# Optimization experiments

Measured on AMD Instinct MI355X. Metric: run time of the kernel, lower is better.

The kernel has to match this reference:

```python
import jax, jax.numpy as jnp
import numpy as np

B, D, H, E = 1024, 64, 128, 8192


def setup_inputs() -> dict:
    key = jax.random.key(0)
    ks = jax.random.split(key, 10)
    def w(k, shape, fan_in):
        return jax.random.normal(k, shape, jnp.float32) / np.float32(np.sqrt(fan_in))
    return {
        "mu": jax.random.normal(ks[0], (B, D), jnp.float32),
        "current_edge_index": jax.random.randint(ks[1], (2, E), 0, B),
        "W1": w(ks[2], (D, H), D),   "b1": jnp.zeros((H,), jnp.float32),
        "W2": w(ks[3], (H, H), H),   "b2": jnp.zeros((H,), jnp.float32),
        "Ws1": w(ks[4], (2 * H, H), 2 * H), "bs1": jnp.zeros((H,), jnp.float32),
        "Ws2": w(ks[5], (H, 1), H),  "bs2": jnp.zeros((1,), jnp.float32),
        "Wg1": w(ks[6], (2 * H, H), 2 * H), "bg1": jnp.zeros((H,), jnp.float32),
        "Wg2": w(ks[7], (H, D), H), "bg2": jnp.zeros((D,), jnp.float32),
    }


def _gcn(x, W, b, src, dst, n):
    loop = jnp.arange(n)
    s = jnp.concatenate([src, loop])
    d = jnp.concatenate([dst, loop])
    deg = jax.ops.segment_sum(jnp.ones_like(s, x.dtype), d, num_segments=n)
    dinv = jax.lax.rsqrt(jnp.maximum(deg, 1e-12))
    norm = dinv[s] * dinv[d]                      # [E+n]
    xw = x @ W                                    # [n,H]
    out = jax.ops.segment_sum(xw[s] * norm[:, None], d, num_segments=n)
    return out + b


def _pairwise_scores(h, Ws1, bs1, Ws2, bs2):
    # score_mlp([h_i || h_j]) for all pairs, vectorized: split first-layer weight
    A = h @ Ws1[:H]                               # [B,H] contribution of h_i
    C = h @ Ws1[H:]                               # [B,H] contribution of h_j
    pre = jax.nn.relu(A[:, None, :] + C[None, :, :] + bs1)   # [B,B,H]
    s = (pre @ Ws2)[..., 0] + bs2[0]              # [B,B]
    up = jnp.triu(s, 1)                           # only i<j computed in original
    return up + up.T                              # symmetric, zero diagonal


def _kruskal(scores_np, n):
    iu, ju = np.triu_indices(n, 1)
    w = scores_np[iu, ju]
    order = np.argsort(-w, kind="stable")         # descending, stable like list.sort
    parent = list(range(n))
    rank = [0] * n
    def find(u):
        while parent[u] != u:
            parent[u] = parent[parent[u]]
            u = parent[u]
        return u
    edges = []
    for k in order:
        i, j = int(iu[k]), int(ju[k])
        ri, rj = find(i), find(j)
        if ri == rj:
            continue
        if rank[ri] < rank[rj]:
            parent[ri] = rj
        elif rank[ri] > rank[rj]:
            parent[rj] = ri
        else:
            parent[rj] = ri
            rank[ri] += 1
        edges.append((i, j))
        if len(edges) == n - 1:
            break
    return np.asarray(edges, dtype=np.int64)      # [n-1, 2]


def reference(mu, current_edge_index, W1, b1, W2, b2, Ws1, bs1, Ws2, bs2, Wg1, bg1, Wg2, bg2):
    src, dst = current_edge_index[0], current_edge_index[1]
    h = jax.nn.relu(_gcn(mu, W1, b1, src, dst, B))
    h = jax.nn.relu(_gcn(h, W2, b2, src, dst, B))
    scores = _pairwise_scores(h, Ws1, bs1, Ws2, bs2)          # [B,B]
    mst = _kruskal(np.asarray(scores), B)                     # [B-1,2], i<j
    ei = jnp.asarray(mst[:, 0])
    ej = jnp.asarray(mst[:, 1])
    # bidirectional edge index: src=[i,j,...], dst=[j,i,...]
    new_edge_index = jnp.stack([
        jnp.stack([ei, ej], axis=1).reshape(-1),
        jnp.stack([ej, ei], axis=1).reshape(-1),
    ], axis=0)                                                # [2, 2*(B-1)]
    hp = jnp.concatenate([h[ei], h[ej]], axis=1)              # [B-1, 2H]
    gamma = jnp.tanh(jax.nn.relu(hp @ Wg1 + bg1) @ Wg2 + bg2) # [B-1, D]
    return (new_edge_index, gamma)
```

## Files before the change

### kernel.cpp

```cpp
#include <hip/hip_runtime.h>
#include <hip/hip_bf16.h>
#include <math.h>

#define BN 1024
#define DIN 64
#define HD 128
#define EN 8192
#define SLOTS_STRIDE 64
#define MMR4 4
#define EGR 8
#define NC 128

typedef unsigned long long u64;

__global__ void k_fill(const int* dst, int* cnt, int* slots) {
    int e = blockIdx.x * blockDim.x + threadIdx.x;
    if (e < EN) {
        int d = dst[e];
        int p = atomicAdd(&cnt[d], 1);
        if (p < SLOTS_STRIDE) slots[d * SLOTS_STRIDE + p] = e;
    }
}

__global__ __launch_bounds__(128) void k_finish(int* slots, const int* cnt, float* dinv) {
    __shared__ int buf[128][65];
    int tid = threadIdx.x;
    int t = blockIdx.x * 128 + tid;
    int n = cnt[t];
    if (n > SLOTS_STRIDE) n = SLOTS_STRIDE;
    for (int k = 0; k < n; k++) buf[tid][k] = slots[t * SLOTS_STRIDE + k];
    for (int k = 1; k < n; k++) {
        int v = buf[tid][k];
        int q = k - 1;
        while (q >= 0 && buf[tid][q] > v) { buf[tid][q + 1] = buf[tid][q]; q--; }
        buf[tid][q + 1] = v;
    }
    for (int k = 0; k < n; k++) slots[t * SLOTS_STRIDE + k] = buf[tid][k];
    dinv[t] = 1.0f / sqrtf(fmaxf((float)(n + 1), 1e-12f));
}

__global__ __launch_bounds__(256) void k_mm4(const float* x, const float* W, const float* bias,
                                             float* out, int K) {
    __shared__ float xr[MMR4][HD];
    int tid = threadIdx.x;
    int r0 = blockIdx.x * MMR4;
    for (int idx = tid; idx < MMR4 * K; idx += 256)
        xr[idx / K][idx % K] = x[r0 * K + idx];
    __syncthreads();
    int col = tid & 127, half = tid >> 7;
    float b = bias ? bias[col] : 0.0f;
    float a0 = b, a1 = b;
#pragma unroll 4
    for (int k = 0; k < K; k++) {
        float w = W[k * HD + col];
        a0 = fmaf(xr[half * 2 + 0][k], w, a0);
        a1 = fmaf(xr[half * 2 + 1][k], w, a1);
    }
    out[(r0 + half * 2 + 0) * HD + col] = a0;
    out[(r0 + half * 2 + 1) * HD + col] = a1;
}

__global__ __launch_bounds__(256) void k_mmAC(const float* h, const float* Ws1, const float* bs1,
                                              float* Aa, float* Cc) {
    __shared__ float xr[MMR4][HD];
    int tid = threadIdx.x;
    int r0 = blockIdx.x * MMR4;
    for (int idx = tid; idx < MMR4 * HD; idx += 256)
        xr[idx >> 7][idx & 127] = h[r0 * HD + idx];
    __syncthreads();
    int col = tid & 127, half = tid >> 7;
    float bc = bs1[col];
    float A0 = 0.0f, A1 = 0.0f, C0 = bc, C1 = bc;
#pragma unroll 2
    for (int k = 0; k < HD; k++) {
        float wa = Ws1[k * HD + col];
        float wc = Ws1[(HD + k) * HD + col];
        A0 = fmaf(xr[half * 2 + 0][k], wa, A0);
        A1 = fmaf(xr[half * 2 + 1][k], wa, A1);
        C0 = fmaf(xr[half * 2 + 0][k], wc, C0);
        C1 = fmaf(xr[half * 2 + 1][k], wc, C1);
    }
    Aa[(r0 + half * 2 + 0) * HD + col] = A0;
    Aa[(r0 + half * 2 + 1) * HD + col] = A1;
    Cc[(r0 + half * 2 + 0) * HD + col] = C0;
    Cc[(r0 + half * 2 + 1) * HD + col] = C1;
}

__global__ __launch_bounds__(128) void k_gather(const float* xw, const float* bvec, const int* src,
                                                const int* slots, const int* cnt,
                                                const float* dinv, float* hout) {
    __shared__ int sn_s[SLOTS_STRIDE];
    __shared__ float w_s[SLOTS_STRIDE];
    int d = blockIdx.x, t = threadIdx.x;
    float dd = dinv[d];
    int n = cnt[d];
    if (n > SLOTS_STRIDE) n = SLOTS_STRIDE;
    if (t < n) {
        int e = slots[d * SLOTS_STRIDE + t];
        int sn = src[e];
        sn_s[t] = sn;
        w_s[t] = dinv[sn] * dd;
    }
    __syncthreads();
    float acc = 0.0f;
    for (int s = 0; s < n; s++)
        acc = fmaf(xw[sn_s[s] * HD + t], w_s[s], acc);
    acc = fmaf(xw[d * HD + t], dd * dd, acc);
    acc += bvec[t];
    hout[d * HD + t] = fmaxf(acc, 0.0f);
}

__device__ __forceinline__ u64 edge_key(float w, int i, int j) {
    unsigned u = __float_as_uint(w);
    u = (u & 0x80000000u) ? ~u : (u | 0x80000000u);
    int a = i < j ? i : j, b = i < j ? j : i;
    unsigned packed = (unsigned)(a * BN + b);
    return ((u64)u << 20) | (u64)(0xFFFFFu - packed);
}

__global__ __launch_bounds__(256) void k_scores(const float* Aa, const float* Cc,
                                                const float* Ws2, const float* bs2v,
                                                float* S, u64* best) {
    int bid = blockIdx.x;
    int bi = 0, rem = bid;
    while (rem >= 16 - bi) { rem -= 16 - bi; bi++; }
    int bj = bi + rem;
    __shared__ float As[64][68];
    __shared__ float Cs[64][68];
    __shared__ float w2[HD];
    __shared__ u64 rmax[64], cmax[64];
    int tid = threadIdx.x;
    int R = bi * 64, Cb = bj * 64;
    if (tid < HD) w2[tid] = Ws2[tid];
    if (tid < 64) { rmax[tid] = 0ull; cmax[tid] = 0ull; }
    int tx = tid & 15, ty = tid >> 4;
    float acc[4][4] = {};
    for (int half = 0; half < 2; half++) {
        int k0 = half * 64;
        __syncthreads();
        for (int idx = tid; idx < 64 * 64; idx += 256) {
            int row = idx >> 6;
            int kk = idx & 63;
            As[kk][row] = Aa[(R + row) * HD + k0 + kk];
            Cs[kk][row] = Cc[(Cb + row) * HD + k0 + kk];
        }
        __syncthreads();
        for (int kk = 0; kk < 64; kk++) {
            float4 av = *(const float4*)&As[kk][ty * 4];
            float4 cv = *(const float4*)&Cs[kk][tx * 4];
            float wk = w2[k0 + kk];
            float ar[4] = {av.x, av.y, av.z, av.w};
            float cr[4] = {cv.x, cv.y, cv.z, cv.w};
#pragma unroll
            for (int r = 0; r < 4; r++)
#pragma unroll
                for (int q = 0; q < 4; q++) {
                    float tv = fmaxf(ar[r] + cr[q], 0.0f);
                    acc[r][q] = fmaf(tv, wk, acc[r][q]);
                }
        }
    }
    float b2 = bs2v[0];
    u64 rloc[4] = {0ull, 0ull, 0ull, 0ull};
    u64 cloc[4] = {0ull, 0ull, 0ull, 0ull};
#pragma unroll
    for (int r = 0; r < 4; r++)
#pragma unroll
        for (int q = 0; q < 4; q++) {
            int gr = R + ty * 4 + r, gc = Cb + tx * 4 + q;
            float v = acc[r][q] + b2;
            if (gr < gc) {
                S[gr * BN + gc] = v;
                S[gc * BN + gr] = v;
                u64 key = edge_key(v, gr, gc);
                if (key > rloc[r]) rloc[r] = key;
                if (key > cloc[q]) cloc[q] = key;
            } else if (gr == gc) S[gr * BN + gc] = 0.0f;
        }
#pragma unroll
    for (int r = 0; r < 4; r++) {
        if (rloc[r]) atomicMax(&rmax[ty * 4 + r], rloc[r]);
        if (cloc[r]) atomicMax(&cmax[tx * 4 + r], cloc[r]);
    }
    __syncthreads();
    if (tid < 64) {
        if (rmax[tid]) atomicMax(&best[R + tid], rmax[tid]);
    } else if (tid < 128) {
        if (cmax[tid - 64]) atomicMax(&best[Cb + tid - 64], cmax[tid - 64]);
    }
}

__global__ __launch_bounds__(256) void k_best(const float* S, const int* comp,
                                              u64* best, const int* mstcnt,
                                              const int* ncompG, int ncGuard) {
    if (*mstcnt >= BN - 1) return;
    if (ncGuard && *ncompG <= NC) return;
    int lane = threadIdx.x & 63;
    int i = blockIdx.x * 4 + (threadIdx.x >> 6);
    int ci = comp[i];
    const float* Srow = S + (size_t)i * BN;
    u64 loc = 0ull;
    for (int j = lane; j < BN; j += 64)
        if (comp[j] != ci) {
            u64 key = edge_key(Srow[j], i, j);
            if (key > loc) loc = key;
        }
#pragma unroll
    for (int off = 32; off > 0; off >>= 1) {
        u64 o = __shfl_xor(loc, off);
        if (o > loc) loc = o;
    }
    if (lane == 0 && loc) atomicMax(&best[ci], loc);
}

__global__ __launch_bounds__(1024) void k_merge1(u64* best, int* comp, u64* mst, int* mstcnt) {
    __shared__ int pa[BN], pb[BN];
    int c = threadIdx.x;
    u64 e = best[c];
    unsigned packed = 0xFFFFFu - (unsigned)(e & 0xFFFFFu);
    int a = packed >> 10, b = packed & 1023;
    int t = (a == c) ? b : a;
    pa[c] = t;
    __syncthreads();
    bool mutual = (pa[t] == c);
    int p0 = pa[c];
    if (mutual && c < t) p0 = c;
    __syncthreads();
    pa[c] = p0;
    __syncthreads();
    if (!(mutual && c > t)) {
        int idx = atomicAdd(mstcnt, 1);
        mst[idx] = e;
    }
    for (int it = 0; it < 10; it++) {
        pb[c] = pa[pa[c]];
        __syncthreads();
        pa[c] = pb[c];
        __syncthreads();
    }
    comp[c] = pa[c];
    best[c] = 0ull;
}

__global__ __launch_bounds__(1024) void k_merge(int* comp, u64* best, u64* mst, int* mstcnt,
                                                int* compD, int* ncompG, int emitDense,
                                                int ncGuard) {
    __shared__ int pa[BN], pb[BN];
    int c = threadIdx.x;
    if (*mstcnt >= BN - 1) return;
    if (ncGuard && *ncompG <= NC) return;
    int myComp = comp[c];
    bool root = (myComp == c);
    u64 e = best[c];
    int t = c;
    if (root && e) {
        unsigned packed = 0xFFFFFu - (unsigned)(e & 0xFFFFFu);
        int a = packed >> 10, b = packed & 1023;
        int ca = comp[a], cb = comp[b];
        t = (ca == c) ? cb : ca;
    }
    pa[c] = (root && e) ? t : c;
    __syncthreads();
    bool mutual = root && e && (pa[t] == c);
    int p0 = pa[c];
    if (mutual && c < t) p0 = c;
    __syncthreads();
    pa[c] = p0;
    __syncthreads();
    if (root && e && !(mutual && c > t)) {
        int idx = atomicAdd(mstcnt, 1);
        mst[idx] = e;
    }
    for (int it = 0; it < 10; it++) {
        pb[c] = pa[pa[c]];
        __syncthreads();
        pa[c] = pb[c];
        __syncthreads();
    }
    comp[c] = pa[myComp];
    best[c] = 0ull;
    if (!emitDense) return;
    __syncthreads();
    int isR = (comp[c] == c) ? 1 : 0;
    pa[c] = isR;
    __syncthreads();
    for (int d = 1; d < BN; d <<= 1) {
        int v = (c >= d) ? pa[c - d] : 0;
        __syncthreads();
        pa[c] += v;
        __syncthreads();
    }
    if (isR) pb[c] = pa[c] - 1;
    __syncthreads();
    compD[c] = pb[comp[c]];
    if (c == BN - 1) *ncompG = pa[BN - 1];
}

__global__ __launch_bounds__(256) void k_Gsp(const float* S, const int* compD,
                                             const int* mstcnt, u64* spG) {
    if (*mstcnt >= BN - 1) return;
    __shared__ u64 t[NC];
    int tid = threadIdx.x;
    int i = blockIdx.x;
    int ci = compD[i];
    if (tid < NC) t[tid] = 0ull;
    __syncthreads();
    const float* Srow = S + (size_t)i * BN;
    for (int j = tid; j < BN; j += 256) {
        int cj = compD[j];
        if (j != i && cj != ci) atomicMax(&t[cj], edge_key(Srow[j], i, j));
    }
    __syncthreads();
    if (tid < NC && t[tid]) atomicMax(&spG[(size_t)ci * NC + tid], t[tid]);
}

struct FinSm {
    union {
        u64 sp[NC][NC];
        u64 sk[BN];
    } u;
    int cnd[BN];
    int ccomp[NC], cpa[NC], cpb[NC];
    u64 cbest[NC];
    int lcnt;
};

__global__ __launch_bounds__(1024) void k_mstfin(const u64* spG, const int* compD,
                                                 const int* ncompG, const int* mstcntG,
                                                 u64* mstG, float* out, int* pairs) {
    __shared__ FinSm sm;
    int c = threadIdx.x;
    int total = *mstcntG;
    if (total < BN - 1) {
        int nc = *ncompG;
        for (int idx = c; idx < NC * NC; idx += 1024) ((u64*)sm.u.sp)[idx] = spG[idx];
        sm.cnd[c] = compD[c];
        if (c < NC) { sm.ccomp[c] = c; sm.cbest[c] = 0ull; }
        if (c == 0) sm.lcnt = 0;
        __syncthreads();
        for (int rr = 0; rr < 8 && total < BN - 1; rr++) {
            if (c < nc) {
                int g = sm.ccomp[c];
                u64 m = 0ull;
                for (int c2 = 0; c2 < nc; c2++)
                    if (sm.ccomp[c2] != g) {
                        u64 v = sm.u.sp[c][c2];
                        if (v > m) m = v;
                    }
                if (m) atomicMax(&sm.cbest[g], m);
            }
            __syncthreads();
            if (c < nc) {
                bool root = (sm.ccomp[c] == c);
                u64 e = sm.cbest[c];
                int t2 = c;
                if (root && e) {
                    unsigned packed = 0xFFFFFu - (unsigned)(e & 0xFFFFFu);
                    int a = packed >> 10, b = packed & 1023;
                    int ga = sm.ccomp[sm.cnd[a]], gb = sm.ccomp[sm.cnd[b]];
                    t2 = (ga == c) ? gb : ga;
                }
                sm.cpa[c] = (root && e) ? t2 : c;
            }
            __syncthreads();
            if (c < nc) {
                bool root = (sm.ccomp[c] == c);
                u64 e = sm.cbest[c];
                int t2 = sm.cpa[c];
                bool mutual = root && e && (sm.cpa[t2] == c);
                int p0 = sm.cpa[c];
                if (mutual && c < t2) p0 = c;
                sm.cpb[c] = p0;
                if (root && e && !(mutual && c > t2)) {
                    int idx = total + atomicAdd(&sm.lcnt, 1);
                    mstG[idx] = e;
                }
            }
            __syncthreads();
            if (c < nc) sm.cpa[c] = sm.cpb[c];
            __syncthreads();
            for (int it = 0; it < 7; it++) {
                if (c < nc) sm.cpb[c] = sm.cpa[sm.cpa[c]];
                __syncthreads();
                if (c < nc) sm.cpa[c] = sm.cpb[c];
                __syncthreads();
            }
            if (c < nc) {
                sm.ccomp[c] = sm.cpa[sm.ccomp[c]];
                sm.cbest[c] = 0ull;
            }
            __syncthreads();
            int added = sm.lcnt;
            __syncthreads();
            total += added;
            if (c == 0) sm.lcnt = 0;
            __syncthreads();
        }
    }
    __syncthreads();
    sm.u.sk[c] = (c < BN - 1) ? mstG[c] : 0ull;
    __syncthreads();
    if (c < BN - 1) {
        u64 mykey = sm.u.sk[c];
        int rk = 0;
        for (int f = 0; f < BN - 1; f++) rk += (sm.u.sk[f] > mykey) ? 1 : 0;
        unsigned packed = 0xFFFFFu - (unsigned)(mykey & 0xFFFFFu);
        int i = packed >> 10, j2 = packed & 1023;
        out[2 * rk] = (float)i;
        out[2 * rk + 1] = (float)j2;
        out[2046 + 2 * rk] = (float)j2;
        out[2046 + 2 * rk + 1] = (float)i;
        pairs[2 * rk] = i;
        pairs[2 * rk + 1] = j2;
    }
}

__global__ __launch_bounds__(256) void k_gamma8(const float* h, const int* pairs,
                                                const float* Wg1, const float* bg1,
                                                const float* Wg2, const float* bg2, float* out) {
    __shared__ float hp[EGR][2 * HD];
    __shared__ float z1[EGR][HD];
    int tid = threadIdx.x;
    int e0 = blockIdx.x * EGR;
    for (int idx = tid; idx < EGR * 2 * HD; idx += 256) {
        int eo = idx >> 8;
        int k = idx & 255;
        int e = e0 + eo;
        if (e < BN - 1) {
            int node = (k < HD) ? pairs[2 * e] : pairs[2 * e + 1];
            hp[eo][k] = h[node * HD + (k & 127)];
        }
    }
    __syncthreads();
    {
        int c = tid & 127, eg = tid >> 7;
        float b = bg1[c];
        float a0 = b, a1 = b, a2 = b, a3 = b;
        for (int k = 0; k < 2 * HD; k++) {
            float w = Wg1[k * HD + c];
            a0 = fmaf(hp[eg * 4 + 0][k], w, a0);
            a1 = fmaf(hp[eg * 4 + 1][k], w, a1);
            a2 = fmaf(hp[eg * 4 + 2][k], w, a2);
            a3 = fmaf(hp[eg * 4 + 3][k], w, a3);
        }
        z1[eg * 4 + 0][c] = fmaxf(a0, 0.0f);
        z1[eg * 4 + 1][c] = fmaxf(a1, 0.0f);
        z1[eg * 4 + 2][c] = fmaxf(a2, 0.0f);
        z1[eg * 4 + 3][c] = fmaxf(a3, 0.0f);
    }
    __syncthreads();
    {
        int co = tid & 63, eh = tid >> 6;
        float b = bg2[co];
        float g0 = b, g1 = b;
        for (int k = 0; k < HD; k++) {
            float w = Wg2[k * DIN + co];
            g0 = fmaf(z1[eh * 2 + 0][k], w, g0);
            g1 = fmaf(z1[eh * 2 + 1][k], w, g1);
        }
        int ea = e0 + eh * 2, eb = ea + 1;
        if (ea < BN - 1) out[4092 + ea * DIN + co] = tanhf(g0);
        if (eb < BN - 1) out[4092 + eb * DIN + co] = tanhf(g1);
    }
}

extern "C" void kernel_launch(void* const* d_in, const int* in_sizes, int n_in,
                              void* d_out, int out_size, void* d_ws, size_t ws_size,
                              hipStream_t stream) {
    const float* mu  = (const float*)d_in[0];
    const int*   ei  = (const int*)d_in[1];
    const float* W1  = (const float*)d_in[2];
    const float* b1  = (const float*)d_in[3];
    const float* W2  = (const float*)d_in[4];
    const float* b2  = (const float*)d_in[5];
    const float* Ws1 = (const float*)d_in[6];
    const float* bs1 = (const float*)d_in[7];
    const float* Ws2 = (const float*)d_in[8];
    const float* bs2 = (const float*)d_in[9];
    const float* Wg1 = (const float*)d_in[10];
    const float* bg1 = (const float*)d_in[11];
    const float* Wg2 = (const float*)d_in[12];
    const float* bg2 = (const float*)d_in[13];
    float* out = (float*)d_out;

    const int* src = ei;
    const int* dst = ei + EN;

    char* ws = (char*)d_ws;
    int*   slots = (int*)(ws);
    float* S     = (float*)(ws);
    float* xw    = (float*)(ws + 4194304);
    float* h1    = (float*)(ws + 4718592);
    float* h2    = (float*)(ws + 5242880);
    float* Aa    = (float*)(ws + 5767168);
    float* Cc    = (float*)(ws + 6291456);
    int*   cnt   = (int*)(ws + 6815744);
    u64*   best  = (u64*)(ws + 6819840);
    int*   mstcnt = (int*)(ws + 6828032);
    u64*   spG   = (u64*)(ws + 6832128);
    int*   comp  = (int*)(ws + 6963200);
    u64*   mstG  = (u64*)(ws + 6967296);
    int*   pairs = (int*)(ws + 6975488);
    int*   compD = (int*)(ws + 6983680);
    int*   ncomp = (int*)(ws + 6987776);
    float* dinv  = (float*)(ws + 6991872);

    hipMemsetAsync(ws + 6815744, 0, 147456, stream);

    k_fill<<<EN / 256, 256, 0, stream>>>(dst, cnt, slots);
    k_finish<<<BN / 128, 128, 0, stream>>>(slots, cnt, dinv);

    k_mm4<<<BN / MMR4, 256, 0, stream>>>(mu, W1, nullptr, xw, DIN);
    k_gather<<<BN, HD, 0, stream>>>(xw, b1, src, slots, cnt, dinv, h1);
    k_mm4<<<BN / MMR4, 256, 0, stream>>>(h1, W2, nullptr, xw, HD);
    k_gather<<<BN, HD, 0, stream>>>(xw, b2, src, slots, cnt, dinv, h2);

    k_mmAC<<<BN / MMR4, 256, 0, stream>>>(h2, Ws1, bs1, Aa, Cc);

    k_scores<<<136, 256, 0, stream>>>(Aa, Cc, Ws2, bs2, S, best);

    k_merge1<<<1, 1024, 0, stream>>>(best, comp, mstG, mstcnt);
    k_best<<<BN / 4, 256, 0, stream>>>(S, comp, best, mstcnt, ncomp, 0);
    k_merge<<<1, 1024, 0, stream>>>(comp, best, mstG, mstcnt, compD, ncomp, 1, 0);
    k_best<<<BN / 4, 256, 0, stream>>>(S, comp, best, mstcnt, ncomp, 1);
    k_merge<<<1, 1024, 0, stream>>>(comp, best, mstG, mstcnt, compD, ncomp, 1, 1);

    k_Gsp<<<BN, 256, 0, stream>>>(S, compD, mstcnt, spG);
    k_mstfin<<<1, 1024, 0, stream>>>(spG, compD, ncomp, mstcnt, mstG, out, pairs);

    k_gamma8<<<(BN - 1 + EGR - 1) / EGR, 256, 0, stream>>>(h2, pairs, Wg1, bg1, Wg2, bg2, out);
}
```

Before: 164.5 us.

## Fuse slot sort with first matmul, stage weights in LDS, vectorize loads, add unrolls

Merges the slot-sorting/degree kernel and the first projection matmul into one launch, with blocks split by role, which removes one launch. The small matmul kernels now copy the full weight matrix into shared memory with float4 loads before computing, and the score tile loads become float4. Several inner loops gain unroll pragmas. Staging the whole weight matrix per block adds a lot of redundant global traffic and LDS pressure: 64-128KB per block for k_mmAC, which may cut occupancy.

```diff
diff --git a/kernel.cpp b/kernel.cpp
--- a/kernel.cpp
+++ b/kernel.cpp
@@ -22,37 +22,71 @@
     }
 }
 
-__global__ __launch_bounds__(128) void k_finish(int* slots, const int* cnt, float* dinv) {
-    __shared__ int buf[128][65];
+struct FinMmSm {
+    union {
+        int buf[256][65];
+        struct { float Wl[DIN * HD]; float xr[MMR4][DIN]; } m;
+    } u;
+};
+__global__ __launch_bounds__(256) void k_finmm1(int* slots, const int* cnt, float* dinv,
+                                                const float* mu, const float* W1, float* xw) {
+    __shared__ FinMmSm sm;
     int tid = threadIdx.x;
-    int t = blockIdx.x * 128 + tid;
-    int n = cnt[t];
-    if (n > SLOTS_STRIDE) n = SLOTS_STRIDE;
-    for (int k = 0; k < n; k++) buf[tid][k] = slots[t * SLOTS_STRIDE + k];
-    for (int k = 1; k < n; k++) {
-        int v = buf[tid][k];
-        int q = k - 1;
-        while (q >= 0 && buf[tid][q] > v) { buf[tid][q + 1] = buf[tid][q]; q--; }
-        buf[tid][q + 1] = v;
-    }
-    for (int k = 0; k < n; k++) slots[t * SLOTS_STRIDE + k] = buf[tid][k];
-    dinv[t] = 1.0f / sqrtf(fmaxf((float)(n + 1), 1e-12f));
-}
-
-__global__ __launch_bounds__(256) void k_mm4(const float* x, const float* W, const float* bias,
-                                             float* out, int K) {
+    if (blockIdx.x < 4) {
+        int t = blockIdx.x * 256 + tid;
+        int n = cnt[t];
+        if (n > SLOTS_STRIDE) n = SLOTS_STRIDE;
+        for (int k = 0; k < n; k++) sm.u.buf[tid][k] = slots[t * SLOTS_STRIDE + k];
+        for (int k = 1; k < n; k++) {
+            int v = sm.u.buf[tid][k];
+            int q = k - 1;
+            while (q >= 0 && sm.u.buf[tid][q] > v) { sm.u.buf[tid][q + 1] = sm.u.buf[tid][q]; q--; }
+            sm.u.buf[tid][q + 1] = v;
+        }
+        for (int k = 0; k < n; k++) slots[t * SLOTS_STRIDE + k] = sm.u.buf[tid][k];
+        dinv[t] = 1.0f / sqrtf(fmaxf((float)(n + 1), 1e-12f));
+    } else {
+        int r0 = (blockIdx.x - 4) * MMR4;
+        for (int idx = tid; idx < DIN * HD / 4; idx += 256)
+            ((float4*)sm.u.m.Wl)[idx] = ((const float4*)W1)[idx];
+        for (int idx = tid; idx < MMR4 * DIN / 4; idx += 256) {
+            float4 v = ((const float4*)(mu + r0 * DIN))[idx];
+            int row = (idx * 4) / DIN, col = (idx * 4) % DIN;
+            sm.u.m.xr[row][col] = v.x; sm.u.m.xr[row][col + 1] = v.y;
+            sm.u.m.xr[row][col + 2] = v.z; sm.u.m.xr[row][col + 3] = v.w;
+        }
+        __syncthreads();
+        int col = tid & 127, half = tid >> 7;
+        float a0 = 0.0f, a1 = 0.0f;
+#pragma unroll 4
+        for (int k = 0; k < DIN; k++) {
+            float w = sm.u.m.Wl[k * HD + col];
+            a0 = fmaf(sm.u.m.xr[half * 2 + 0][k], w, a0);
+            a1 = fmaf(sm.u.m.xr[half * 2 + 1][k], w, a1);
+        }
+        xw[(r0 + half * 2 + 0) * HD + col] = a0;
+        xw[(r0 + half * 2 + 1) * HD + col] = a1;
+    }
+}
+
+__global__ __launch_bounds__(256) void k_mm128(const float* x, const float* W, float* out) {
+    __shared__ float Wl[HD * HD];
     __shared__ float xr[MMR4][HD];
     int tid = threadIdx.x;
     int r0 = blockIdx.x * MMR4;
-    for (int idx = tid; idx < MMR4 * K; idx += 256)
-        xr[idx / K][idx % K] = x[r0 * K + idx];
+    for (int idx = tid; idx < HD * HD / 4; idx += 256)
+        ((float4*)Wl)[idx] = ((const float4*)W)[idx];
+    for (int idx = tid; idx < MMR4 * HD / 4; idx += 256) {
+        float4 v = ((const float4*)(x + r0 * HD))[idx];
+        int row = idx >> 5, col = (idx & 31) * 4;
+        xr[row][col] = v.x; xr[row][col + 1] = v.y; xr[row][col + 2] = v.z; xr[row][col + 3] = v.w;
+    }
     __syncthreads();
     int col = tid & 127, half = tid >> 7;
-    float b = bias ? bias[col] : 0.0f;
-    float a0 = b, a1 = b;
+    float a0 = 0.0f, a1 = 0.0f;
 #pragma unroll 4
-    for (int k = 0; k < K; k++) {
-        float w = W[k * HD + col];
+    for (int k = 0; k < HD; k++) {
+        float w = Wl[k * HD + col];
         a0 = fmaf(xr[half * 2 + 0][k], w, a0);
         a1 = fmaf(xr[half * 2 + 1][k], w, a1);
     }
@@ -62,19 +96,25 @@
 
 __global__ __launch_bounds__(256) void k_mmAC(const float* h, const float* Ws1, const float* bs1,
                                               float* Aa, float* Cc) {
+    __shared__ float Wl[2 * HD * HD];
     __shared__ float xr[MMR4][HD];
     int tid = threadIdx.x;
     int r0 = blockIdx.x * MMR4;
-    for (int idx = tid; idx < MMR4 * HD; idx += 256)
-        xr[idx >> 7][idx & 127] = h[r0 * HD + idx];
+    for (int idx = tid; idx < 2 * HD * HD / 4; idx += 256)
+        ((float4*)Wl)[idx] = ((const float4*)Ws1)[idx];
+    for (int idx = tid; idx < MMR4 * HD / 4; idx += 256) {
+        float4 v = ((const float4*)(h + r0 * HD))[idx];
+        int row = idx >> 5, col = (idx & 31) * 4;
+        xr[row][col] = v.x; xr[row][col + 1] = v.y; xr[row][col + 2] = v.z; xr[row][col + 3] = v.w;
+    }
     __syncthreads();
     int col = tid & 127, half = tid >> 7;
     float bc = bs1[col];
     float A0 = 0.0f, A1 = 0.0f, C0 = bc, C1 = bc;
 #pragma unroll 2
     for (int k = 0; k < HD; k++) {
-        float wa = Ws1[k * HD + col];
-        float wc = Ws1[(HD + k) * HD + col];
+        float wa = Wl[k * HD + col];
+        float wc = Wl[(HD + k) * HD + col];
         A0 = fmaf(xr[half * 2 + 0][k], wa, A0);
         A1 = fmaf(xr[half * 2 + 1][k], wa, A1);
         C0 = fmaf(xr[half * 2 + 0][k], wc, C0);
@@ -103,6 +143,7 @@
     }
     __syncthreads();
     float acc = 0.0f;
+#pragma unroll 4
     for (int s = 0; s < n; s++)
         acc = fmaf(xw[sn_s[s] * HD + t], w_s[s], acc);
     acc = fmaf(xw[d * HD + t], dd * dd, acc);
@@ -138,11 +179,14 @@
     for (int half = 0; half < 2; half++) {
         int k0 = half * 64;
         __syncthreads();
-        for (int idx = tid; idx < 64 * 64; idx += 256) {
-            int row = idx >> 6;
-            int kk = idx & 63;
-            As[kk][row] = Aa[(R + row) * HD + k0 + kk];
-            Cs[kk][row] = Cc[(Cb + row) * HD + k0 + kk];
+        for (int f = tid; f < 1024; f += 256) {
+            int row = f >> 4, kk4 = (f & 15) * 4;
+            float4 a = *(const float4*)&Aa[(R + row) * HD + k0 + kk4];
+            float4 c = *(const float4*)&Cc[(Cb + row) * HD + k0 + kk4];
+            As[kk4 + 0][row] = a.x; As[kk4 + 1][row] = a.y;
+            As[kk4 + 2][row] = a.z; As[kk4 + 3][row] = a.w;
+            Cs[kk4 + 0][row] = c.x; Cs[kk4 + 1][row] = c.y;
+            Cs[kk4 + 2][row] = c.z; Cs[kk4 + 3][row] = c.w;
         }
         __syncthreads();
         for (int kk = 0; kk < 64; kk++) {
@@ -200,6 +244,7 @@
     int ci = comp[i];
     const float* Srow = S + (size_t)i * BN;
     u64 loc = 0ull;
+#pragma unroll 4
     for (int j = lane; j < BN; j += 64)
         if (comp[j] != ci) {
             u64 key = edge_key(Srow[j], i, j);
@@ -306,6 +351,7 @@
     if (tid < NC) t[tid] = 0ull;
     __syncthreads();
     const float* Srow = S + (size_t)i * BN;
+#pragma unroll 2
     for (int j = tid; j < BN; j += 256) {
         int cj = compD[j];
         if (j != i && cj != ci) atomicMax(&t[cj], edge_key(Srow[j], i, j));
@@ -436,6 +482,7 @@
         int c = tid & 127, eg = tid >> 7;
         float b = bg1[c];
         float a0 = b, a1 = b, a2 = b, a3 = b;
+#pragma unroll 4
         for (int k = 0; k < 2 * HD; k++) {
             float w = Wg1[k * HD + c];
             a0 = fmaf(hp[eg * 4 + 0][k], w, a0);
@@ -453,6 +500,7 @@
         int co = tid & 63, eh = tid >> 6;
         float b = bg2[co];
         float g0 = b, g1 = b;
+#pragma unroll 4
         for (int k = 0; k < HD; k++) {
             float w = Wg2[k * DIN + co];
             g0 = fmaf(z1[eh * 2 + 0][k], w, g0);
@@ -508,11 +556,9 @@
     hipMemsetAsync(ws + 6815744, 0, 147456, stream);
 
     k_fill<<<EN / 256, 256, 0, stream>>>(dst, cnt, slots);
-    k_finish<<<BN / 128, 128, 0, stream>>>(slots, cnt, dinv);
-
-    k_mm4<<<BN / MMR4, 256, 0, stream>>>(mu, W1, nullptr, xw, DIN);
+    k_finmm1<<<260, 256, 0, stream>>>(slots, cnt, dinv, mu, W1, xw);
     k_gather<<<BN, HD, 0, stream>>>(xw, b1, src, slots, cnt, dinv, h1);
-    k_mm4<<<BN / MMR4, 256, 0, stream>>>(h1, W2, nullptr, xw, HD);
+    k_mm128<<<BN / MMR4, 256, 0, stream>>>(h1, W2, xw);
     k_gather<<<BN, HD, 0, stream>>>(xw, b2, src, slots, cnt, dinv, h2);
 
     k_mmAC<<<BN / MMR4, 256, 0, stream>>>(h2, Ws1, bs1, Aa, Cc);
```

Measured after the change: 155.9 us. 1.05x faster.
